# Optimization experiments

Measured on AMD Instinct MI355X. Metric: run time of the kernel, lower is better.

## Reference

```python
import jax, jax.numpy as jnp
import numpy as np

N0, K3, K2 = 262144, 27, 8
N1, N2 = N0 // 8, N0 // 64
CIN, C0, C1, C2 = 3, 24, 48, 96
EPS = 1e-5


def _conv_bn_relu(x, neigh, W, gamma, beta):
    # Octree sparse conv: gather neighbor features and contract with kernel.
    # x: [N, Cin], neigh: [M, K] int indices into N, W: [K, Cin, Cout]
    y = jnp.einsum('mkc,kcd->md', x[neigh], W)
    # BatchNorm1d (training-mode batch statistics) + ReLU
    mu = jnp.mean(y, axis=0)
    var = jnp.var(y, axis=0)
    y = (y - mu) * jax.lax.rsqrt(var + EPS) * gamma + beta
    return jax.nn.relu(y)


def setup_inputs() -> dict:
    key = jax.random.key(0)
    k = jax.random.split(key, 16)

    def w(kk, shape, fan):
        return jax.random.normal(kk, shape, jnp.float32) / np.float32(np.sqrt(fan))

    return {
        'data':   jax.random.normal(k[0], (N0, CIN), jnp.float32),
        'neigh0': jax.random.randint(k[1], (N0, K3), 0, N0, jnp.int32),
        'child0': jax.random.randint(k[2], (N1, K2), 0, N0, jnp.int32),
        'neigh1': jax.random.randint(k[3], (N1, K3), 0, N1, jnp.int32),
        'child1': jax.random.randint(k[4], (N2, K2), 0, N1, jnp.int32),
        'neigh2': jax.random.randint(k[5], (N2, K3), 0, N2, jnp.int32),
        'w0':  w(k[6],  (K3, CIN, C0), K3 * CIN),
        'g0':  jnp.ones((C0,), jnp.float32),  'b0':  jnp.zeros((C0,), jnp.float32),
        'wd0': w(k[7],  (K2, C0, C1),  K2 * C0),
        'gd0': jnp.ones((C1,), jnp.float32),  'bd0': jnp.zeros((C1,), jnp.float32),
        'w1':  w(k[8],  (K3, C1, C1),  K3 * C1),
        'g1':  jnp.ones((C1,), jnp.float32),  'b1':  jnp.zeros((C1,), jnp.float32),
        'wd1': w(k[9],  (K2, C1, C2),  K2 * C1),
        'gd1': jnp.ones((C2,), jnp.float32),  'bd1': jnp.zeros((C2,), jnp.float32),
        'wp':  w(k[10], (K3, C2, C2),  K3 * C2),
        'gp':  jnp.ones((C2,), jnp.float32),  'bp':  jnp.zeros((C2,), jnp.float32),
    }


def reference(data, neigh0, child0, neigh1, child1, neigh2,
              w0, g0, b0, wd0, gd0, bd0, w1, g1, b1, wd1, gd1, bd1, wp, gp, bp):
    # stage 0 at depth d: conv3 then stride-2 downsample
    x = _conv_bn_relu(data, neigh0, w0, g0, b0)      # [N0, 24]
    x = _conv_bn_relu(x, child0, wd0, gd0, bd0)      # [N1, 48]
    # stage 1 at depth d-1
    x = _conv_bn_relu(x, neigh1, w1, g1, b1)         # [N1, 48]
    x = _conv_bn_relu(x, child1, wd1, gd1, bd1)      # [N2, 96]
    # proj at depth d-2
    x = _conv_bn_relu(x, neigh2, wp, gp, bp)         # [N2, 96]
    return x
```

## Files before the change

kernel.cpp:

```cpp
#include <hip/hip_runtime.h>

#define N0 262144
#define N1 32768
#define N2 4096
#define EPSBN 1e-5f

typedef unsigned short ush_t;
typedef __bf16 bf16x8 __attribute__((ext_vector_type(8)));
typedef float  f32x4  __attribute__((ext_vector_type(4)));

union ufcast { unsigned int u; float f; };
__device__ __forceinline__ float bflo(unsigned int p) { ufcast x; x.u = p << 16;          return x.f; }
__device__ __forceinline__ float bfhi(unsigned int p) { ufcast x; x.u = p & 0xffff0000u; return x.f; }
__device__ __forceinline__ ush_t f2bf(float f) {
    ufcast x; x.f = f;
    unsigned int u = x.u + 0x7fffu + ((x.u >> 16) & 1u);
    return (ush_t)(u >> 16);
}
__device__ __forceinline__ bf16x8 as_bf8(uint4 u) {
    union { uint4 u; bf16x8 b; } x; x.u = u; return x.b;
}

template<int C>
__device__ __forceinline__ void compute_ss(const float* __restrict__ bins,
                                           const float* __restrict__ g, const float* __restrict__ b,
                                           float M, float* ssl)
{
    const int tid = threadIdx.x;
    if (tid < 2 * C) {
        float s = 0.f;
#pragma unroll
        for (int k = 0; k < 16; ++k) s += bins[k * 2 * C + tid];
        ssl[tid] = s;
    }
    __syncthreads();
    if (tid < C) {
        const float mu  = ssl[tid] / M;
        const float var = fmaxf(ssl[C + tid] / M - mu * mu, 0.f);
        const float sc  = g[tid] / sqrtf(var + EPSBN);
        const float sh  = b[tid] - mu * sc;
        ssl[tid] = sc; ssl[C + tid] = sh;
    }
    __syncthreads();
}

template<int K, int CIN, int CINP_W, int COUT, int COUTP, int NCH>
__device__ __forceinline__ void prep_stage(const float* __restrict__ W, ush_t* __restrict__ Wb, int e) {
    const int k  = e & 31;
    const int n  = (e >> 5) % COUTP;
    const int ch = e / (32 * COUTP);
    const int kp = ch * 32 + k;
    const int t  = kp / CINP_W;
    const int c  = kp % CINP_W;
    float v = 0.f;
    if (t < K && c < CIN && n < COUT) v = W[((size_t)t * CIN + c) * COUT + n];
    Wb[e] = f2bf(v);
}

__global__ __launch_bounds__(256) void prep_all(
    const float* w0, const float* wd0, const float* w1, const float* wd1, const float* wp,
    const float* data,
    ush_t* wbA, ush_t* wbB, ush_t* wbC, ush_t* wbD, ush_t* wbE, ush_t* xa)
{
    const int e = blockIdx.x * 256 + threadIdx.x;
    switch (blockIdx.y) {
        case 0: if (e <   4096) prep_stage<27,  3,  4, 24, 32,  4>(w0,  wbA, e); break;
        case 1: if (e <  12288) prep_stage< 8, 24, 32, 48, 48,  8>(wd0, wbB, e); break;
        case 2: if (e <  82944) prep_stage<27, 48, 64, 48, 48, 54>(w1,  wbC, e); break;
        case 3: if (e <  49152) prep_stage< 8, 48, 64, 96, 96, 16>(wd1, wbD, e); break;
        case 4: if (e < 248832) prep_stage<27, 96, 96, 96, 96, 81>(wp,  wbE, e); break;
        case 5: if (e < N0) {
            const float* dp = data + (size_t)3 * e;
            unsigned int h0 = f2bf(dp[0]), h1 = f2bf(dp[1]), h2 = f2bf(dp[2]);
            uint2 v; v.x = h0 | (h1 << 16); v.y = h2;
            ((uint2*)xa)[e] = v;
        } break;
    }
}

__global__ __launch_bounds__(256) void mconvA_s(
    const ush_t* __restrict__ xa,
    const int*   __restrict__ neigh,
    const ush_t* __restrict__ Wb,
    ush_t*       __restrict__ y,
    float*       __restrict__ bins)
{
    __shared__ int nl[64][29];
    __shared__ float lsq[48];
    const int tid = threadIdx.x;
    const int block0 = blockIdx.x * 64;

    for (int i = tid; i < 64 * 27; i += 256)
        nl[i / 27][i % 27] = neigh[(size_t)block0 * 27 + i];
    if (tid < 48) lsq[tid] = 0.f;
    __syncthreads();

    const int lane = tid & 63, wave = tid >> 6;
    const int quad = lane >> 4, l15 = lane & 15;
    const int lr = wave * 16 + l15;

    f32x4 acc[2] = {};
#pragma unroll
    for (int ch = 0; ch < 4; ++ch) {
        const int tA = ch * 8 + quad * 2;
        uint4 au = make_uint4(0, 0, 0, 0);
        if (ch < 3) {
            const uint2 lo = ((const uint2*)xa)[nl[lr][tA]];
            const uint2 hi = ((const uint2*)xa)[nl[lr][tA + 1]];
            au = make_uint4(lo.x, lo.y, hi.x, hi.y);
        } else {
            if (quad == 0) {
                const uint2 lo = ((const uint2*)xa)[nl[lr][24]];
                const uint2 hi = ((const uint2*)xa)[nl[lr][25]];
                au = make_uint4(lo.x, lo.y, hi.x, hi.y);
            } else if (quad == 1) {
                const uint2 lo = ((const uint2*)xa)[nl[lr][26]];
                au = make_uint4(lo.x, lo.y, 0, 0);
            }
        }
        const bf16x8 af = as_bf8(au);
#pragma unroll
        for (int ct = 0; ct < 2; ++ct) {
            const int n = ct * 16 + l15;
            const uint4 bu = *(const uint4*)(Wb + ((size_t)ch * 32 + n) * 32 + quad * 8);
            acc[ct] = __builtin_amdgcn_mfma_f32_16x16x32_bf16(af, as_bf8(bu), acc[ct], 0, 0, 0);
        }
    }

#pragma unroll
    for (int ct = 0; ct < 2; ++ct) {
        const int col = ct * 16 + l15;
        if (col < 24) {
            float s = 0.f, q = 0.f;
#pragma unroll
            for (int r = 0; r < 4; ++r) {
                const float v = acc[ct][r];
                const int rr = block0 + wave * 16 + quad * 4 + r;
                y[(size_t)rr * 24 + col] = f2bf(v);
                s += v; q += v * v;
            }
            atomicAdd(&lsq[col], s);
            atomicAdd(&lsq[24 + col], q);
        }
    }
    __syncthreads();
    if (tid < 48) atomicAdd(&bins[(blockIdx.x & 15) * 48 + tid], lsq[tid]);
}

__global__ __launch_bounds__(256) void mconvB_s(
    const ush_t* __restrict__ y0,
    const float* __restrict__ bins0,
    const float* __restrict__ g, const float* __restrict__ b,
    const int*   __restrict__ child,
    const ush_t* __restrict__ Wb,
    float*       __restrict__ y1,
    float*       __restrict__ bins1)
{
    __shared__ float ssl[48];
    __shared__ float lsq[96];
    const int tid = threadIdx.x;
    if (tid < 96) lsq[tid] = 0.f;
    compute_ss<24>(bins0, g, b, (float)N0, ssl);

    const int lane = tid & 63, wave = tid >> 6;
    const int quad = lane >> 4, l15 = lane & 15;
    const int rowA = blockIdx.x * 64 + wave * 16 + l15;
    const int c0 = quad * 8;

    float sc[8], sh[8];
    if (c0 < 24) {
#pragma unroll
        for (int j = 0; j < 8; ++j) { sc[j] = ssl[c0 + j]; sh[j] = ssl[24 + c0 + j]; }
    }

    f32x4 acc[3] = {};
#pragma unroll
    for (int ci = 0; ci < 8; ++ci) {
        const int idx = child[(size_t)rowA * 8 + ci];
        uint4 au = make_uint4(0, 0, 0, 0);
        if (c0 < 24) {
            const uint4 raw = *(const uint4*)(y0 + (size_t)idx * 24 + c0);
            const unsigned int w4[4] = {raw.x, raw.y, raw.z, raw.w};
            unsigned int o4[4];
#pragma unroll
            for (int h = 0; h < 4; ++h) {
                const float a0 = fmaxf(bflo(w4[h]) * sc[2 * h]     + sh[2 * h],     0.f);
                const float a1 = fmaxf(bfhi(w4[h]) * sc[2 * h + 1] + sh[2 * h + 1], 0.f);
                o4[h] = (unsigned)f2bf(a0) | ((unsigned)f2bf(a1) << 16);
            }
            au = make_uint4(o4[0], o4[1], o4[2], o4[3]);
        }
        const bf16x8 af = as_bf8(au);
#pragma unroll
        for (int ct = 0; ct < 3; ++ct) {
            const int n = ct * 16 + l15;
            const uint4 bu = *(const uint4*)(Wb + ((size_t)ci * 48 + n) * 32 + quad * 8);
            acc[ct] = __builtin_amdgcn_mfma_f32_16x16x32_bf16(af, as_bf8(bu), acc[ct], 0, 0, 0);
        }
    }

#pragma unroll
    for (int ct = 0; ct < 3; ++ct) {
        const int col = ct * 16 + l15;
        float s = 0.f, q = 0.f;
#pragma unroll
        for (int r = 0; r < 4; ++r) {
            const float v = acc[ct][r];
            const int rr = blockIdx.x * 64 + wave * 16 + quad * 4 + r;
            y1[(size_t)rr * 48 + col] = v;
            s += v; q += v * v;
        }
        atomicAdd(&lsq[col], s);
        atomicAdd(&lsq[48 + col], q);
    }
    __syncthreads();
    if (tid < 96) atomicAdd(&bins1[(blockIdx.x & 15) * 96 + tid], lsq[tid]);
}

__global__ __launch_bounds__(256) void actC_s(
    const float* __restrict__ y1, const float* __restrict__ bins1,
    const float* __restrict__ g, const float* __restrict__ b,
    ush_t* __restrict__ xb)
{
    __shared__ float ssl[96];
    compute_ss<48>(bins1, g, b, (float)N1, ssl);

    const int i = (blockIdx.x * 256 + threadIdx.x) * 4;
    const int c = i % 64;
    ushort4 o;
    if (c >= 48) {
        o.x = o.y = o.z = o.w = 0;
    } else {
        const int r = i / 64;
        float4 v = *(const float4*)(y1 + (size_t)r * 48 + c);
        o.x = f2bf(fmaxf(v.x * ssl[c + 0] + ssl[48 + c + 0], 0.f));
        o.y = f2bf(fmaxf(v.y * ssl[c + 1] + ssl[48 + c + 1], 0.f));
        o.z = f2bf(fmaxf(v.z * ssl[c + 2] + ssl[48 + c + 2], 0.f));
        o.w = f2bf(fmaxf(v.w * ssl[c + 3] + ssl[48 + c + 3], 0.f));
    }
    *(ushort4*)(xb + i) = o;
}

__global__ __launch_bounds__(256) void mconvC_s(
    const ush_t* __restrict__ xb,
    const int*   __restrict__ neigh,
    const ush_t* __restrict__ Wb,
    float*       __restrict__ y2,
    float*       __restrict__ bins2)
{
    __shared__ float lsq[96];
    const int tid = threadIdx.x;
    if (tid < 96) lsq[tid] = 0.f;
    __syncthreads();

    const int lane = tid & 63, wave = tid >> 6;
    const int quad = lane >> 4, l15 = lane & 15;
    const int rowA = blockIdx.x * 64 + wave * 16 + l15;

    f32x4 acc[3] = {};
#pragma unroll 6
    for (int ch = 0; ch < 54; ++ch) {
        const int t = ch >> 1, sub = ch & 1;
        const int idx = neigh[(size_t)rowA * 27 + t];
        const uint4 au = *(const uint4*)(xb + (size_t)idx * 64 + sub * 32 + quad * 8);
        const bf16x8 af = as_bf8(au);
#pragma unroll
        for (int ct = 0; ct < 3; ++ct) {
            const int n = ct * 16 + l15;
            const uint4 bu = *(const uint4*)(Wb + ((size_t)ch * 48 + n) * 32 + quad * 8);
            acc[ct] = __builtin_amdgcn_mfma_f32_16x16x32_bf16(af, as_bf8(bu), acc[ct], 0, 0, 0);
        }
    }

#pragma unroll
    for (int ct = 0; ct < 3; ++ct) {
        const int col = ct * 16 + l15;
        float s = 0.f, q = 0.f;
#pragma unroll
        for (int r = 0; r < 4; ++r) {
            const float v = acc[ct][r];
            const int rr = blockIdx.x * 64 + wave * 16 + quad * 4 + r;
            y2[(size_t)rr * 48 + col] = v;
            s += v; q += v * v;
        }
        atomicAdd(&lsq[col], s);
        atomicAdd(&lsq[48 + col], q);
    }
    __syncthreads();
    if (tid < 96) atomicAdd(&bins2[(blockIdx.x & 15) * 96 + tid], lsq[tid]);
}

__global__ __launch_bounds__(256) void mconvD_s(
    const float* __restrict__ y2, const float* __restrict__ bins2,
    const float* __restrict__ g, const float* __restrict__ b,
    const int*   __restrict__ child,
    const ush_t* __restrict__ Wb,
    float*       __restrict__ y3,
    float*       __restrict__ bins3)
{
    __shared__ float ssl[96];
    __shared__ float tile[16 * 96];
    const int tid = threadIdx.x;
    for (int i = tid; i < 1536; i += 256) tile[i] = 0.f;
    compute_ss<48>(bins2, g, b, (float)N1, ssl);

    const int lane = tid & 63, wave = tid >> 6;
    const int quad = lane >> 4, l15 = lane & 15;
    const int rowA = blockIdx.x * 16 + l15;

    f32x4 acc[6] = {};
#pragma unroll
    for (int u = 0; u < 4; ++u) {
        const int ci = wave * 4 + u;
        const int t = ci >> 1, sub = ci & 1;
        const int idx = child[(size_t)rowA * 8 + t];
        const int c0 = sub * 32 + quad * 8;
        uint4 au = make_uint4(0, 0, 0, 0);
        if (c0 < 48) {
            const float4 v0 = *(const float4*)(y2 + (size_t)idx * 48 + c0);
            const float4 v1 = *(const float4*)(y2 + (size_t)idx * 48 + c0 + 4);
            const float vv[8] = {v0.x, v0.y, v0.z, v0.w, v1.x, v1.y, v1.z, v1.w};
            unsigned int o4[4];
#pragma unroll
            for (int h = 0; h < 4; ++h) {
                const float a0 = fmaxf(vv[2 * h]     * ssl[c0 + 2 * h]     + ssl[48 + c0 + 2 * h],     0.f);
                const float a1 = fmaxf(vv[2 * h + 1] * ssl[c0 + 2 * h + 1] + ssl[48 + c0 + 2 * h + 1], 0.f);
                o4[h] = (unsigned)f2bf(a0) | ((unsigned)f2bf(a1) << 16);
            }
            au = make_uint4(o4[0], o4[1], o4[2], o4[3]);
        }
        const bf16x8 af = as_bf8(au);
#pragma unroll
        for (int ct = 0; ct < 6; ++ct) {
            const int n = ct * 16 + l15;
            const uint4 bu = *(const uint4*)(Wb + ((size_t)ci * 96 + n) * 32 + quad * 8);
            acc[ct] = __builtin_amdgcn_mfma_f32_16x16x32_bf16(af, as_bf8(bu), acc[ct], 0, 0, 0);
        }
    }

#pragma unroll
    for (int ct = 0; ct < 6; ++ct)
#pragma unroll
        for (int r = 0; r < 4; ++r)
            atomicAdd(&tile[(quad * 4 + r) * 96 + ct * 16 + l15], acc[ct][r]);
    __syncthreads();

    const size_t row0 = (size_t)blockIdx.x * 16;
    for (int i = tid; i < 1536; i += 256) y3[row0 * 96 + i] = tile[i];
    if (tid < 96) {
        float s = 0.f, q = 0.f;
#pragma unroll
        for (int r = 0; r < 16; ++r) { const float v = tile[r * 96 + tid]; s += v; q += v * v; }
        atomicAdd(&bins3[(blockIdx.x & 15) * 192 + tid], s);
        atomicAdd(&bins3[(blockIdx.x & 15) * 192 + 96 + tid], q);
    }
}

__global__ __launch_bounds__(256) void mconvE_s(
    const float* __restrict__ y3, const float* __restrict__ bins3,
    const float* __restrict__ g, const float* __restrict__ b,
    const int*   __restrict__ neigh,
    const ush_t* __restrict__ Wb,
    float*       __restrict__ y4,
    float*       __restrict__ bins4)
{
    __shared__ float ssl[192];
    __shared__ float tile[16 * 96];
    const int tid = threadIdx.x;
    for (int i = tid; i < 1536; i += 256) tile[i] = 0.f;
    compute_ss<96>(bins3, g, b, (float)N2, ssl);

    const int lane = tid & 63, wave = tid >> 6;
    const int quad = lane >> 4, l15 = lane & 15;
    const int rowA = blockIdx.x * 16 + l15;

    const int ci0 = (wave == 0) ? 0 : 21 + (wave - 1) * 20;
    const int cnt = (wave == 0) ? 21 : 20;

    f32x4 acc[6] = {};
    for (int u = 0; u < cnt; ++u) {
        const int ci = ci0 + u;
        const int t = ci / 3, sub = ci % 3;
        const int idx = neigh[(size_t)rowA * 27 + t];
        const int c0 = sub * 32 + quad * 8;
        const float4 v0 = *(const float4*)(y3 + (size_t)idx * 96 + c0);
        const float4 v1 = *(const float4*)(y3 + (size_t)idx * 96 + c0 + 4);
        const float vv[8] = {v0.x, v0.y, v0.z, v0.w, v1.x, v1.y, v1.z, v1.w};
        unsigned int o4[4];
#pragma unroll
        for (int h = 0; h < 4; ++h) {
            const float a0 = fmaxf(vv[2 * h]     * ssl[c0 + 2 * h]     + ssl[96 + c0 + 2 * h],     0.f);
            const float a1 = fmaxf(vv[2 * h + 1] * ssl[c0 + 2 * h + 1] + ssl[96 + c0 + 2 * h + 1], 0.f);
            o4[h] = (unsigned)f2bf(a0) | ((unsigned)f2bf(a1) << 16);
        }
        const bf16x8 af = as_bf8(make_uint4(o4[0], o4[1], o4[2], o4[3]));
#pragma unroll
        for (int ct = 0; ct < 6; ++ct) {
            const int n = ct * 16 + l15;
            const uint4 bu = *(const uint4*)(Wb + ((size_t)ci * 96 + n) * 32 + quad * 8);
            acc[ct] = __builtin_amdgcn_mfma_f32_16x16x32_bf16(af, as_bf8(bu), acc[ct], 0, 0, 0);
        }
    }

#pragma unroll
    for (int ct = 0; ct < 6; ++ct)
#pragma unroll
        for (int r = 0; r < 4; ++r)
            atomicAdd(&tile[(quad * 4 + r) * 96 + ct * 16 + l15], acc[ct][r]);
    __syncthreads();

    const size_t row0 = (size_t)blockIdx.x * 16;
    for (int i = tid; i < 1536; i += 256) y4[row0 * 96 + i] = tile[i];
    if (tid < 96) {
        float s = 0.f, q = 0.f;
#pragma unroll
        for (int r = 0; r < 16; ++r) { const float v = tile[r * 96 + tid]; s += v; q += v * v; }
        atomicAdd(&bins4[(blockIdx.x & 15) * 192 + tid], s);
        atomicAdd(&bins4[(blockIdx.x & 15) * 192 + 96 + tid], q);
    }
}

__global__ __launch_bounds__(256) void writeout_s(
    const float* __restrict__ y4, const float* __restrict__ bins4,
    const float* __restrict__ g, const float* __restrict__ b,
    float* __restrict__ out)
{
    __shared__ float ssl[192];
    compute_ss<96>(bins4, g, b, (float)N2, ssl);

    const int i = (blockIdx.x * 256 + threadIdx.x) * 4;
    const int c = i % 96;
    float4 v = *(const float4*)(y4 + i);
    float4 o;
    o.x = fmaxf(v.x * ssl[c + 0] + ssl[96 + c + 0], 0.f);
    o.y = fmaxf(v.y * ssl[c + 1] + ssl[96 + c + 1], 0.f);
    o.z = fmaxf(v.z * ssl[c + 2] + ssl[96 + c + 2], 0.f);
    o.w = fmaxf(v.w * ssl[c + 3] + ssl[96 + c + 3], 0.f);
    *(float4*)(out + i) = o;
}

extern "C" void kernel_launch(void* const* d_in, const int* in_sizes, int n_in,
                              void* d_out, int out_size, void* d_ws, size_t ws_size,
                              hipStream_t stream)
{
    const float* data   = (const float*)d_in[0];
    const int*   neigh0 = (const int*)d_in[1];
    const int*   child0 = (const int*)d_in[2];
    const int*   neigh1 = (const int*)d_in[3];
    const int*   child1 = (const int*)d_in[4];
    const int*   neigh2 = (const int*)d_in[5];
    const float* w0  = (const float*)d_in[6];
    const float* g0  = (const float*)d_in[7];
    const float* b0  = (const float*)d_in[8];
    const float* wd0 = (const float*)d_in[9];
    const float* gd0 = (const float*)d_in[10];
    const float* bd0 = (const float*)d_in[11];
    const float* w1  = (const float*)d_in[12];
    const float* g1  = (const float*)d_in[13];
    const float* b1  = (const float*)d_in[14];
    const float* wd1 = (const float*)d_in[15];
    const float* gd1 = (const float*)d_in[16];
    const float* bd1 = (const float*)d_in[17];
    const float* wp  = (const float*)d_in[18];
    const float* gp  = (const float*)d_in[19];
    const float* bp  = (const float*)d_in[20];
    float* out = (float*)d_out;

    float* wsf = (float*)d_ws;
    float* bins0 = wsf;
    float* bins1 = wsf + 768;
    float* bins2 = wsf + 2304;
    float* bins3 = wsf + 3840;
    float* bins4 = wsf + 6912;

    float* Y1  = wsf + 10240;
    float* Y2  = Y1 + (size_t)1572864;
    float* Y3  = Y2 + (size_t)1572864;
    float* Y4  = Y3 + (size_t)393216;
    ush_t* Y0B = (ush_t*)(Y4 + (size_t)393216);
    ush_t* XB  = Y0B + (size_t)6291456;
    ush_t* XA  = XB + (size_t)2097152;
    ush_t* WB  = XA + (size_t)1048576;

    ush_t* wbA = WB;
    ush_t* wbB = WB + 4096;
    ush_t* wbC = WB + 16384;
    ush_t* wbD = WB + 99328;
    ush_t* wbE = WB + 148480;

    hipMemsetAsync(d_ws, 0, 9984 * sizeof(float), stream);

    prep_all<<<dim3(1024, 6), 256, 0, stream>>>(w0, wd0, w1, wd1, wp, data,
                                                wbA, wbB, wbC, wbD, wbE, XA);

    mconvA_s<<<N0 / 64, 256, 0, stream>>>(XA, neigh0, wbA, Y0B, bins0);
    mconvB_s<<<N1 / 64, 256, 0, stream>>>(Y0B, bins0, g0, b0, child0, wbB, Y1, bins1);
    actC_s  <<<N1 * 64 / 4 / 256, 256, 0, stream>>>(Y1, bins1, gd0, bd0, XB);
    mconvC_s<<<N1 / 64, 256, 0, stream>>>(XB, neigh1, wbC, Y2, bins2);
    mconvD_s<<<N2 / 16, 256, 0, stream>>>(Y2, bins2, g1, b1, child1, wbD, Y3, bins3);
    mconvE_s<<<N2 / 16, 256, 0, stream>>>(Y3, bins3, gd1, bd1, neigh2, wbE, Y4, bins4);
    writeout_s<<<N2 * 96 / 4 / 256, 256, 0, stream>>>(Y4, bins4, gp, bp, out);

    (void)in_sizes; (void)n_in; (void)out_size; (void)ws_size;
}
```

Before: 260.1 us.

## Fuse BN+ReLU of stage-1 input into conv gather and drop channel padding

Removes the separate actC_s activation kernel. mconvB now stores its raw output as bf16 with 48 channels, and mconvC applies the batch-norm scale/shift and ReLU on the fly to each gathered neighbour row before the MFMA. The K dimension is repacked from 64-padded (54 chunks) to a dense 48 per tap (42 chunks), which cuts gather bytes and MFMA work. In exchange the normalisation arithmetic is repeated for every gathered neighbour, and the pre-BN values are rounded to bf16 before normalisation.

```diff
diff --git a/kernel.cpp b/kernel.cpp
--- a/kernel.cpp
+++ b/kernel.cpp
@@ -66,7 +66,7 @@
     switch (blockIdx.y) {
         case 0: if (e <   4096) prep_stage<27,  3,  4, 24, 32,  4>(w0,  wbA, e); break;
         case 1: if (e <  12288) prep_stage< 8, 24, 32, 48, 48,  8>(wd0, wbB, e); break;
-        case 2: if (e <  82944) prep_stage<27, 48, 64, 48, 48, 54>(w1,  wbC, e); break;
+        case 2: if (e <  64512) prep_stage<27, 48, 48, 48, 48, 42>(w1,  wbC, e); break;
         case 3: if (e <  49152) prep_stage< 8, 48, 64, 96, 96, 16>(wd1, wbD, e); break;
         case 4: if (e < 248832) prep_stage<27, 96, 96, 96, 96, 81>(wp,  wbE, e); break;
         case 5: if (e < N0) {
@@ -153,7 +153,7 @@
     const float* __restrict__ g, const float* __restrict__ b,
     const int*   __restrict__ child,
     const ush_t* __restrict__ Wb,
-    float*       __restrict__ y1,
+    ush_t*       __restrict__ y1b,
     float*       __restrict__ bins1)
 {
     __shared__ float ssl[48];
@@ -207,7 +207,7 @@
         for (int r = 0; r < 4; ++r) {
             const float v = acc[ct][r];
             const int rr = blockIdx.x * 64 + wave * 16 + quad * 4 + r;
-            y1[(size_t)rr * 48 + col] = v;
+            y1b[(size_t)rr * 48 + col] = f2bf(v);
             s += v; q += v * v;
         }
         atomicAdd(&lsq[col], s);
@@ -217,58 +217,60 @@
     if (tid < 96) atomicAdd(&bins1[(blockIdx.x & 15) * 96 + tid], lsq[tid]);
 }
 
-__global__ __launch_bounds__(256) void actC_s(
-    const float* __restrict__ y1, const float* __restrict__ bins1,
+__global__ __launch_bounds__(256) void mconvC_s(
+    const ush_t* __restrict__ y1b,
+    const float* __restrict__ bins1,
     const float* __restrict__ g, const float* __restrict__ b,
-    ush_t* __restrict__ xb)
-{
-    __shared__ float ssl[96];
-    compute_ss<48>(bins1, g, b, (float)N1, ssl);
-
-    const int i = (blockIdx.x * 256 + threadIdx.x) * 4;
-    const int c = i % 64;
-    ushort4 o;
-    if (c >= 48) {
-        o.x = o.y = o.z = o.w = 0;
-    } else {
-        const int r = i / 64;
-        float4 v = *(const float4*)(y1 + (size_t)r * 48 + c);
-        o.x = f2bf(fmaxf(v.x * ssl[c + 0] + ssl[48 + c + 0], 0.f));
-        o.y = f2bf(fmaxf(v.y * ssl[c + 1] + ssl[48 + c + 1], 0.f));
-        o.z = f2bf(fmaxf(v.z * ssl[c + 2] + ssl[48 + c + 2], 0.f));
-        o.w = f2bf(fmaxf(v.w * ssl[c + 3] + ssl[48 + c + 3], 0.f));
-    }
-    *(ushort4*)(xb + i) = o;
-}
-
-__global__ __launch_bounds__(256) void mconvC_s(
-    const ush_t* __restrict__ xb,
     const int*   __restrict__ neigh,
     const ush_t* __restrict__ Wb,
     float*       __restrict__ y2,
     float*       __restrict__ bins2)
 {
+    __shared__ float ssl[96];
     __shared__ float lsq[96];
     const int tid = threadIdx.x;
     if (tid < 96) lsq[tid] = 0.f;
-    __syncthreads();
+    compute_ss<48>(bins1, g, b, (float)N1, ssl);
 
     const int lane = tid & 63, wave = tid >> 6;
     const int quad = lane >> 4, l15 = lane & 15;
     const int rowA = blockIdx.x * 64 + wave * 16 + l15;
 
+    int coffs[3], tofs[3];
+    float sc[3][8], sh[3][8];
+#pragma unroll
+    for (int m3 = 0; m3 < 3; ++m3) {
+        const int gg = 32 * m3 + 8 * quad;
+        coffs[m3] = gg % 48;
+        tofs[m3]  = gg / 48;
+#pragma unroll
+        for (int j = 0; j < 8; ++j) { sc[m3][j] = ssl[coffs[m3] + j]; sh[m3][j] = ssl[48 + coffs[m3] + j]; }
+    }
+
     f32x4 acc[3] = {};
-#pragma unroll 6
-    for (int ch = 0; ch < 54; ++ch) {
-        const int t = ch >> 1, sub = ch & 1;
-        const int idx = neigh[(size_t)rowA * 27 + t];
-        const uint4 au = *(const uint4*)(xb + (size_t)idx * 64 + sub * 32 + quad * 8);
-        const bf16x8 af = as_bf8(au);
-#pragma unroll
-        for (int ct = 0; ct < 3; ++ct) {
-            const int n = ct * 16 + l15;
-            const uint4 bu = *(const uint4*)(Wb + ((size_t)ch * 48 + n) * 32 + quad * 8);
-            acc[ct] = __builtin_amdgcn_mfma_f32_16x16x32_bf16(af, as_bf8(bu), acc[ct], 0, 0, 0);
+    for (int cg = 0; cg < 14; ++cg) {
+#pragma unroll
+        for (int m3 = 0; m3 < 3; ++m3) {
+            const int ch = 3 * cg + m3;
+            int t = 2 * cg + tofs[m3];
+            if (t > 26) t = 26;
+            const int idx = neigh[(size_t)rowA * 27 + t];
+            const uint4 raw = *(const uint4*)(y1b + (size_t)idx * 48 + coffs[m3]);
+            const unsigned int w4[4] = {raw.x, raw.y, raw.z, raw.w};
+            unsigned int o4[4];
+#pragma unroll
+            for (int h = 0; h < 4; ++h) {
+                const float a0 = fmaxf(bflo(w4[h]) * sc[m3][2 * h]     + sh[m3][2 * h],     0.f);
+                const float a1 = fmaxf(bfhi(w4[h]) * sc[m3][2 * h + 1] + sh[m3][2 * h + 1], 0.f);
+                o4[h] = (unsigned)f2bf(a0) | ((unsigned)f2bf(a1) << 16);
+            }
+            const bf16x8 af = as_bf8(make_uint4(o4[0], o4[1], o4[2], o4[3]));
+#pragma unroll
+            for (int ct = 0; ct < 3; ++ct) {
+                const int n = ct * 16 + l15;
+                const uint4 bu = *(const uint4*)(Wb + ((size_t)ch * 48 + n) * 32 + quad * 8);
+                acc[ct] = __builtin_amdgcn_mfma_f32_16x16x32_bf16(af, as_bf8(bu), acc[ct], 0, 0, 0);
+            }
         }
     }
 
@@ -473,20 +475,19 @@
     float* bins3 = wsf + 3840;
     float* bins4 = wsf + 6912;
 
-    float* Y1  = wsf + 10240;
-    float* Y2  = Y1 + (size_t)1572864;
+    float* Y2  = wsf + 10240;
     float* Y3  = Y2 + (size_t)1572864;
     float* Y4  = Y3 + (size_t)393216;
     ush_t* Y0B = (ush_t*)(Y4 + (size_t)393216);
-    ush_t* XB  = Y0B + (size_t)6291456;
-    ush_t* XA  = XB + (size_t)2097152;
+    ush_t* Y1B = Y0B + (size_t)6291456;
+    ush_t* XA  = Y1B + (size_t)1572864;
     ush_t* WB  = XA + (size_t)1048576;
 
     ush_t* wbA = WB;
     ush_t* wbB = WB + 4096;
     ush_t* wbC = WB + 16384;
-    ush_t* wbD = WB + 99328;
-    ush_t* wbE = WB + 148480;
+    ush_t* wbD = WB + 80896;
+    ush_t* wbE = WB + 130048;
 
     hipMemsetAsync(d_ws, 0, 9984 * sizeof(float), stream);
 
@@ -494,9 +495,8 @@
                                                 wbA, wbB, wbC, wbD, wbE, XA);
 
     mconvA_s<<<N0 / 64, 256, 0, stream>>>(XA, neigh0, wbA, Y0B, bins0);
-    mconvB_s<<<N1 / 64, 256, 0, stream>>>(Y0B, bins0, g0, b0, child0, wbB, Y1, bins1);
-    actC_s  <<<N1 * 64 / 4 / 256, 256, 0, stream>>>(Y1, bins1, gd0, bd0, XB);
-    mconvC_s<<<N1 / 64, 256, 0, stream>>>(XB, neigh1, wbC, Y2, bins2);
+    mconvB_s<<<N1 / 64, 256, 0, stream>>>(Y0B, bins0, g0, b0, child0, wbB, Y1B, bins1);
+    mconvC_s<<<N1 / 64, 256, 0, stream>>>(Y1B, bins1, gd0, bd0, neigh1, wbC, Y2, bins2);
     mconvD_s<<<N2 / 16, 256, 0, stream>>>(Y2, bins2, g1, b1, child1, wbD, Y3, bins3);
     mconvE_s<<<N2 / 16, 256, 0, stream>>>(Y3, bins3, gd1, bd1, neigh2, wbE, Y4, bins4);
     writeout_s<<<N2 * 96 / 4 / 256, 256, 0, stream>>>(Y4, bins4, gp, bp, out);
```

Result: faster. 254.0 us (-2.3%).
